# Performance work log

Measured on AMD Instinct MI355X. Metric: run time of the kernel, lower is better.

Reference implementation:

```python
import jax, jax.numpy as jnp
import numpy as np

N, D = 8192, 128
EPS = 1e-6  # torch F.pairwise_distance default eps


def _pe(d, s=3, t=2):
    # 1/d^s - 1/d^t
    return 1.0 / (d ** s) - 1.0 / (d ** t)


def setup_inputs() -> dict:
    key = jax.random.key(0)
    x = jax.random.normal(key, (N, D), dtype=jnp.float32)
    return {"x": x}


def reference(x):
    n = x.shape[0]
    # loss0: distance of each row to the origin; torch pairwise_distance adds eps to the diff
    d0 = jnp.sqrt(jnp.sum((x + EPS) ** 2, axis=-1))  # [N]
    loss0 = jnp.mean(jnp.clip(_pe(d0), -1.5, 1000.0))

    # pdist: condensed upper-triangular pairwise Euclidean distances (no eps)
    sq = jnp.sum(x * x, axis=-1)                      # [N]
    d2 = sq[:, None] + sq[None, :] - 2.0 * (x @ x.T)  # [N, N]
    mask = jnp.triu(jnp.ones((n, n), dtype=bool), k=1)
    # keep masked entries at 1.0 so sqrt/pe stay finite
    d2 = jnp.where(mask, jnp.maximum(d2, 0.0), 1.0)
    d = jnp.sqrt(d2)
    vals = jnp.clip(_pe(d), -1.5, 1000.0)
    cnt = n * (n - 1) // 2
    loss = jnp.sum(jnp.where(mask, vals, 0.0)) / cnt
    return loss0 + loss
```

## Files before the change

### kernel.cpp

```cpp
#include <hip/hip_runtime.h>
#include <hip/hip_bf16.h>


#define NROWS 8192
#define DDIM  128
#define TILE  128
#define RB    128
#define TTILES (NROWS / TILE)
#define NTRI  (TTILES * (TTILES + 1) / 2)
#define NBLKP 1024
#define NCVT  1024
#define FEPS  1e-6f

typedef float f32x4 __attribute__((ext_vector_type(4)));
typedef float f32x2 __attribute__((ext_vector_type(2)));
typedef long long i64;

__device__ __forceinline__ float rsq_fast(float x) {
    float r;
    asm("v_rsq_f32 %0, %1" : "=v"(r) : "v"(x));
    return r;
}
__device__ __forceinline__ f32x2 pk_fma(f32x2 a, f32x2 b, f32x2 c) {
    f32x2 d;
    asm("v_pk_fma_f32 %0, %1, %2, %3" : "=v"(d) : "v"(a), "v"(b), "v"(c));
    return d;
}
__device__ __forceinline__ f32x2 pk_add(f32x2 a, f32x2 b) {
    f32x2 d;
    asm("v_pk_add_f32 %0, %1, %2" : "=v"(d) : "v"(a), "v"(b));
    return d;
}
__device__ __forceinline__ f32x2 pk_mul(f32x2 a, f32x2 b) {
    f32x2 d;
    asm("v_pk_mul_f32 %0, %1, %2" : "=v"(d) : "v"(a), "v"(b));
    return d;
}

__global__ __launch_bounds__(256) void convert_kernel(
        const float* __restrict__ x, unsigned int* __restrict__ xf8_u32,
        float* __restrict__ sq, float* __restrict__ p0) {
    int tid = threadIdx.x;
    int idx = blockIdx.x * 256 + tid;
    int row = idx >> 5, sub = idx & 31;

    float4 v = *(const float4*)(x + (size_t)row * DDIM + sub * 4);
    float s = v.x * v.x + v.y * v.y + v.z * v.z + v.w * v.w;
    float ex = v.x + FEPS, ey = v.y + FEPS, ez = v.z + FEPS, ew = v.w + FEPS;
    float e = ex * ex + ey * ey + ez * ez + ew * ew;

    int p01 = __builtin_amdgcn_cvt_pk_fp8_f32(v.x, v.y, 0, false);
    int p23 = __builtin_amdgcn_cvt_pk_fp8_f32(v.z, v.w, 0, false);
    xf8_u32[(size_t)row * 32 + sub] =
        (unsigned)(p01 & 0xFFFF) | ((unsigned)(p23 & 0xFFFF) << 16);

    #pragma unroll
    for (int off = 16; off; off >>= 1) {
        s += __shfl_down(s, off, 32);
        e += __shfl_down(e, off, 32);
    }

    __shared__ float red[8];
    if (sub == 0) {
        sq[row] = s;
        float r = rsq_fast(e);
        float r2 = r * r;
        red[tid >> 5] = fminf(fmaxf(r2 * r - r2, -1.5f), 1000.0f);
    }
    __syncthreads();
    if (tid == 0) {
        float t = 0.f;
        #pragma unroll
        for (int w = 0; w < 8; ++w) t += red[w];
        p0[blockIdx.x] = t;
    }
}

__device__ __forceinline__ int tri_off(int i) {
    return i * TTILES - ((i * (i - 1)) >> 1);
}

__device__ __forceinline__ void stage_tile(const char* __restrict__ g,
                                           char* lds, int tid) {
    uint4 v[2];
    #pragma unroll
    for (int p = 0; p < 2; ++p)
        v[p] = *(const uint4*)(g + (p * 512 + tid) * 16);
    #pragma unroll
    for (int p = 0; p < 2; ++p) {
        int n = p * 512 + tid;
        int row = n >> 3, c = n & 7;
        *(uint4*)(lds + row * RB + ((c * 16) ^ ((row & 7) << 4))) = v[p];
    }
}

__global__ __launch_bounds__(512, 4) void pair_kernel(
        const unsigned int* __restrict__ xf8_u32,
        const float* __restrict__ sq, float* __restrict__ pp) {
    const char* xb = (const char*)xf8_u32;
    __shared__ char smem[32768];
    char* ldsA = smem;
    char* ldsB = smem + 16384;

    int b = blockIdx.x;
    int t0, cnt;
    if (b < 32) { t0 = b * 3; cnt = 3; }
    else        { t0 = 96 + (b - 32) * 2; cnt = 2; }

    int I = 0;
    {
        float T2 = 2.0f * TTILES + 1.0f;
        I = (int)((T2 - sqrtf(T2 * T2 - 8.0f * (float)t0)) * 0.5f);
        while (tri_off(I + 1) <= t0) ++I;
        while (tri_off(I) > t0) --I;
    }
    int J = I + (t0 - tri_off(I));

    int tid = threadIdx.x;
    int wave = tid >> 6, lane = tid & 63;
    int wR = (wave >> 2) * 64;
    int wC = (wave & 3) * 32;
    int lcol = lane & 15;
    int lrow = lane >> 4;

    const f32x2 neg2 = {-2.0f, -2.0f};
    f32x2 l3 = {0.f, 0.f}, l2 = {0.f, 0.f};
    float ldiag = 0.0f;
    f32x2 si2[4][2];
    int curI = -1;

    for (int k = 0; k < cnt; ++k) {
        if (I != curI) {
            stage_tile(xb + (size_t)I * TILE * RB, ldsA, tid);
            int ibase = I * TILE + wR + lrow * 4;
            #pragma unroll
            for (int r = 0; r < 4; ++r)
                #pragma unroll
                for (int h = 0; h < 2; ++h) {
                    float2 v = *(const float2*)(sq + ibase + r * 16 + h * 2);
                    si2[r][h] = (f32x2){v.x, v.y};
                }
            curI = I;
        }
        bool diag = (I == J);
        if (!diag) stage_tile(xb + (size_t)J * TILE * RB, ldsB, tid);
        __syncthreads();
        const char* bufB = diag ? ldsA : ldsB;

        f32x4 acc[4][2];
        #pragma unroll
        for (int r = 0; r < 4; ++r)
            #pragma unroll
            for (int c = 0; c < 2; ++c) acc[r][c] = (f32x4){0.f, 0.f, 0.f, 0.f};

        #pragma unroll
        for (int ks = 0; ks < 4; ++ks) {
            int koff = ks * 32 + lrow * 8;
            i64 a[4], bb[2];
            #pragma unroll
            for (int r = 0; r < 4; ++r) {
                int row = wR + r * 16 + lcol;
                a[r] = *(const i64*)(ldsA + row * RB + (koff ^ ((row & 7) << 4)));
            }
            #pragma unroll
            for (int c = 0; c < 2; ++c) {
                int row = wC + c * 16 + lcol;
                bb[c] = *(const i64*)(bufB + row * RB + (koff ^ ((row & 7) << 4)));
            }
            #pragma unroll
            for (int r = 0; r < 4; ++r)
                #pragma unroll
                for (int c = 0; c < 2; ++c)
                    acc[r][c] = __builtin_amdgcn_mfma_f32_16x16x32_fp8_fp8(
                        a[r], bb[c], acc[r][c], 0, 0, 0);
        }

        int jbase = J * TILE + wC + lcol;
        float sqj[2];
        #pragma unroll
        for (int c = 0; c < 2; ++c) sqj[c] = sq[jbase + c * 16];

        if (!diag) {
            f32x2 sj2[2];
            #pragma unroll
            for (int c = 0; c < 2; ++c) sj2[c] = (f32x2){sqj[c], sqj[c]};
            #pragma unroll
            for (int r = 0; r < 4; ++r)
                #pragma unroll
                for (int c = 0; c < 2; ++c) {
                    const f32x2* accp = (const f32x2*)&acc[r][c];
                    #pragma unroll
                    for (int h = 0; h < 2; ++h) {
                        f32x2 acc2 = accp[h];
                        f32x2 s2 = pk_add(si2[r][h], sj2[c]);
                        f32x2 d2 = pk_fma(acc2, neg2, s2);
                        f32x2 rv = {rsq_fast(d2[0]), rsq_fast(d2[1])};
                        f32x2 r2 = pk_mul(rv, rv);
                        l3 = pk_fma(r2, rv, l3);
                        l2 = pk_add(l2, r2);
                    }
                }
        } else {
            int il0 = wR + lrow * 4;
            int jl0 = wC + lcol;
            #pragma unroll
            for (int r = 0; r < 4; ++r)
                #pragma unroll
                for (int u = 0; u < 4; ++u) {
                    int il = il0 + r * 16 + u;
                    float si = si2[r][u >> 1][u & 1];
                    #pragma unroll
                    for (int c = 0; c < 2; ++c) {
                        if (jl0 + c * 16 > il) {
                            float d2 = fmaxf(si + sqj[c] - 2.0f * acc[r][c][u], 1e-30f);
                            float rv = rsq_fast(d2);
                            float r2 = rv * rv;
                            ldiag += fminf(r2 * rv - r2, 1000.0f);
                        }
                    }
                }
        }
        __syncthreads();

        ++J;
        if (J == TTILES) { ++I; J = I; }
    }

    float lsum = (l3[0] + l3[1]) - (l2[0] + l2[1]) + ldiag;

    #pragma unroll
    for (int off = 32; off; off >>= 1) lsum += __shfl_down(lsum, off);
    __shared__ float red[8];
    if (lane == 0) red[wave] = lsum;
    __syncthreads();
    if (tid == 0) {
        float t = 0.f;
        #pragma unroll
        for (int w = 0; w < 8; ++w) t += red[w];
        pp[blockIdx.x] = t;
    }
}

__global__ __launch_bounds__(1024) void reduce_kernel(
        const float* __restrict__ p0, int n0,
        const float* __restrict__ pp, int np, float* __restrict__ out) {
    int tid = threadIdx.x;
    double s0 = 0.0, sp = 0.0;
    for (int i = tid; i < n0; i += 1024) s0 += (double)p0[i];
    for (int i = tid; i < np; i += 1024) sp += (double)pp[i];
    #pragma unroll
    for (int off = 32; off; off >>= 1) {
        s0 += __shfl_down(s0, off);
        sp += __shfl_down(sp, off);
    }
    __shared__ double sh[32];
    int wave = tid >> 6, lane = tid & 63;
    if (lane == 0) { sh[2 * wave] = s0; sh[2 * wave + 1] = sp; }
    __syncthreads();
    if (tid == 0) {
        double a = 0.0, bsum = 0.0;
        #pragma unroll
        for (int w = 0; w < 16; ++w) { a += sh[2 * w]; bsum += sh[2 * w + 1]; }
        double cnt = (double)NROWS * (double)(NROWS - 1) * 0.5;
        out[0] = (float)(a / (double)NROWS + bsum / cnt);
    }
}

extern "C" void kernel_launch(void* const* d_in, const int* in_sizes, int n_in,
                              void* d_out, int out_size, void* d_ws, size_t ws_size,
                              hipStream_t stream) {
    const float* x = (const float*)d_in[0];
    char* ws = (char*)d_ws;
    const size_t OFF_SQ = 1048576;
    const size_t OFF_P0 = OFF_SQ + 32768;
    const size_t OFF_PP = OFF_P0 + 8192;
    if (ws_size < OFF_PP + NBLKP * sizeof(float)) return;

    unsigned int* xf8 = (unsigned int*)ws;
    float* sq = (float*)(ws + OFF_SQ);
    float* p0 = (float*)(ws + OFF_P0);
    float* pp = (float*)(ws + OFF_PP);

    convert_kernel<<<NCVT, 256, 0, stream>>>(x, xf8, sq, p0);
    pair_kernel<<<NBLKP, 512, 0, stream>>>(xf8, sq, pp);
    reduce_kernel<<<1, 1024, 0, stream>>>(p0, NCVT, pp, NBLKP, (float*)d_out);
}
```

Measured before the change: 28.95 us.

## Prefetch next tile pair into registers while computing current tile

Global loads of the next I/J tiles are now issued into registers before the MFMA loop for the current tile and written to LDS at the start of the next iteration. The swizzled LDS offsets are precomputed once per thread, and the tile index advance moves ahead of the compute so the correct J is kept in curJ. The aim is to hide global-memory latency behind the matrix math. The cost is extra live registers (two uint4 pairs) under a 512x4 launch bound, which could cause spills, and each block only processes 2-3 tiles, so there is little to overlap.

```diff
diff --git a/kernel.cpp b/kernel.cpp
--- a/kernel.cpp
+++ b/kernel.cpp
@@ -80,20 +80,6 @@
     return i * TTILES - ((i * (i - 1)) >> 1);
 }
 
-__device__ __forceinline__ void stage_tile(const char* __restrict__ g,
-                                           char* lds, int tid) {
-    uint4 v[2];
-    #pragma unroll
-    for (int p = 0; p < 2; ++p)
-        v[p] = *(const uint4*)(g + (p * 512 + tid) * 16);
-    #pragma unroll
-    for (int p = 0; p < 2; ++p) {
-        int n = p * 512 + tid;
-        int row = n >> 3, c = n & 7;
-        *(uint4*)(lds + row * RB + ((c * 16) ^ ((row & 7) << 4))) = v[p];
-    }
-}
-
 __global__ __launch_bounds__(512, 4) void pair_kernel(
         const unsigned int* __restrict__ xf8_u32,
         const float* __restrict__ sq, float* __restrict__ pp) {
@@ -123,15 +109,39 @@
     int lcol = lane & 15;
     int lrow = lane >> 4;
 
+    int wofs[2];
+    #pragma unroll
+    for (int p = 0; p < 2; ++p) {
+        int n = p * 512 + tid;
+        int row = n >> 3, c = n & 7;
+        wofs[p] = row * RB + ((c * 16) ^ ((row & 7) << 4));
+    }
+
     const f32x2 neg2 = {-2.0f, -2.0f};
     f32x2 l3 = {0.f, 0.f}, l2 = {0.f, 0.f};
     float ldiag = 0.0f;
     f32x2 si2[4][2];
+
+    uint4 regA[2], regB[2];
+    bool haveA = true, haveB = (I != J);
+    {
+        const char* gA = xb + (size_t)I * TILE * RB;
+        #pragma unroll
+        for (int p = 0; p < 2; ++p)
+            regA[p] = *(const uint4*)(gA + (p * 512 + tid) * 16);
+        if (haveB) {
+            const char* gB = xb + (size_t)J * TILE * RB;
+            #pragma unroll
+            for (int p = 0; p < 2; ++p)
+                regB[p] = *(const uint4*)(gB + (p * 512 + tid) * 16);
+        }
+    }
     int curI = -1;
 
     for (int k = 0; k < cnt; ++k) {
-        if (I != curI) {
-            stage_tile(xb + (size_t)I * TILE * RB, ldsA, tid);
+        if (haveA) {
+            #pragma unroll
+            for (int p = 0; p < 2; ++p) *(uint4*)(ldsA + wofs[p]) = regA[p];
             int ibase = I * TILE + wR + lrow * 4;
             #pragma unroll
             for (int r = 0; r < 4; ++r)
@@ -143,9 +153,34 @@
             curI = I;
         }
         bool diag = (I == J);
-        if (!diag) stage_tile(xb + (size_t)J * TILE * RB, ldsB, tid);
+        if (haveB) {
+            #pragma unroll
+            for (int p = 0; p < 2; ++p) *(uint4*)(ldsB + wofs[p]) = regB[p];
+        }
+        const char* bufB = diag ? ldsA : ldsB;
+        int curJ = J;
+
+        ++J;
+        if (J == TTILES) { ++I; J = I; }
+        haveA = false; haveB = false;
+        if (k + 1 < cnt) {
+            if (I != curI) {
+                const char* gA = xb + (size_t)I * TILE * RB;
+                #pragma unroll
+                for (int p = 0; p < 2; ++p)
+                    regA[p] = *(const uint4*)(gA + (p * 512 + tid) * 16);
+                haveA = true;
+            }
+            if (I != J) {
+                const char* gB = xb + (size_t)J * TILE * RB;
+                #pragma unroll
+                for (int p = 0; p < 2; ++p)
+                    regB[p] = *(const uint4*)(gB + (p * 512 + tid) * 16);
+                haveB = true;
+            }
+        }
+
         __syncthreads();
-        const char* bufB = diag ? ldsA : ldsB;
 
         f32x4 acc[4][2];
         #pragma unroll
@@ -175,7 +210,7 @@
                         a[r], bb[c], acc[r][c], 0, 0, 0);
         }
 
-        int jbase = J * TILE + wC + lcol;
+        int jbase = curJ * TILE + wC + lcol;
         float sqj[2];
         #pragma unroll
         for (int c = 0; c < 2; ++c) sqj[c] = sq[jbase + c * 16];
@@ -221,9 +256,6 @@
                 }
         }
         __syncthreads();
-
-        ++J;
-        if (J == TTILES) { ++I; J = I; }
     }
 
     float lsum = (l3[0] + l3[1]) - (l2[0] + l2[1]) + ldiag;
```

Result: slower. 38.72 us (+33.8%).
